# Kernel optimization log

Hardware: AMD Instinct MI355X
Metric: run time of the kernel (lower is better)

## Reference

```python
import jax, jax.numpy as jnp
import numpy as np

B, S, D, H = 2, 2048, 1024, 16
DK = D // H


def setup_inputs() -> dict:
    key = jax.random.key(0)
    ks = jax.random.split(key, 10)
    scale = 1.0 / np.sqrt(D)
    x = jax.random.normal(ks[0], (B, S, D), dtype=jnp.float32)
    # causal mask: 1 = attend, 0 = masked (module's create_causal_mask)
    mask = jnp.tril(jnp.ones((S, S), dtype=jnp.int32))[None, None]
    Wq = jax.random.normal(ks[1], (D, D), jnp.float32) * scale
    bq = jax.random.normal(ks[2], (D,), jnp.float32) * 0.01
    Wk = jax.random.normal(ks[3], (D, D), jnp.float32) * scale
    bk = jax.random.normal(ks[4], (D,), jnp.float32) * 0.01
    Wv = jax.random.normal(ks[5], (D, D), jnp.float32) * scale
    bv = jax.random.normal(ks[6], (D,), jnp.float32) * 0.01
    Wo = jax.random.normal(ks[7], (D, D), jnp.float32) * scale
    bo = jax.random.normal(ks[8], (D,), jnp.float32) * 0.01
    return {"x": x, "mask": mask, "Wq": Wq, "bq": bq, "Wk": Wk, "bk": bk,
            "Wv": Wv, "bv": bv, "Wo": Wo, "bo": bo}


def reference(x, mask, Wq, bq, Wk, bk, Wv, bv, Wo, bo):
    b, s, _ = x.shape
    # projections; [B,S,D] -> [B,H,S,DK]
    def split_heads(t):
        return t.reshape(b, s, H, DK).transpose(0, 2, 1, 3)
    Q = split_heads(x @ Wq + bq)
    K = split_heads(x @ Wk + bk)
    V = split_heads(x @ Wv + bv)
    scores = jnp.einsum('bhqd,bhkd->bhqk', Q, K) / np.sqrt(DK)
    scores = jnp.where(mask == 0, jnp.float32(-1e9), scores)
    attn = jax.nn.softmax(scores, axis=-1)  # dropout p=0 -> identity
    ctx = jnp.einsum('bhqk,bhkd->bhqd', attn, V)
    ctx = ctx.transpose(0, 2, 1, 3).reshape(b, s, D)
    return ctx @ Wo + bo
```

## Files before the change

### kernel.cpp

```cpp
#include <hip/hip_runtime.h>
#include <hip/hip_bf16.h>


typedef _Float16 f16x8 __attribute__((ext_vector_type(8)));
typedef _Float16 f16x4 __attribute__((ext_vector_type(4)));
typedef _Float16 f16x2 __attribute__((ext_vector_type(2)));
typedef float f32x4 __attribute__((ext_vector_type(4)));

#define QSCALE 0.180336880111112f

__device__ __forceinline__ void async_copy16(const _Float16* gsrc,
                                             _Float16* ldst) {
  __builtin_amdgcn_global_load_lds(
      (const __attribute__((address_space(1))) void*)gsrc,
      (__attribute__((address_space(3))) void*)ldst, 16, 0, 0);
}

__global__ __launch_bounds__(256) void prep(
    const float* __restrict__ x, _Float16* __restrict__ xh,
    const float* __restrict__ W0, const float* __restrict__ W1,
    const float* __restrict__ W2, const float* __restrict__ W3,
    _Float16* __restrict__ T0, _Float16* __restrict__ T1,
    _Float16* __restrict__ T2, _Float16* __restrict__ T3) {
  if (blockIdx.x < 4096) {
    int i = (blockIdx.x * 256 + threadIdx.x) * 4;
    float4 v = *(const float4*)(x + i);
    f16x4 o;
    o.x = (_Float16)v.x; o.y = (_Float16)v.y;
    o.z = (_Float16)v.z; o.w = (_Float16)v.w;
    *(f16x4*)(xh + i) = o;
    return;
  }
  const int id = blockIdx.x - 4096;
  const int w = id >> 10, rem = id & 1023;
  const int bx = rem & 31, by = rem >> 5;
  const float* W; _Float16* T;
  switch (w) {
    case 0: W = W0; T = T0; break;
    case 1: W = W1; T = T1; break;
    case 2: W = W2; T = T2; break;
    default: W = W3; T = T3; break;
  }
  __shared__ _Float16 tile[32][33];
  const int tx = threadIdx.x & 31, ty = threadIdx.x >> 5;
  const int n0 = bx * 32, k0 = by * 32;
  for (int i = 0; i < 4; i++) {
    int kk = k0 + ty + i * 8;
    tile[ty + i * 8][tx] = (_Float16)W[(size_t)kk * 1024 + n0 + tx];
  }
  __syncthreads();
  for (int i = 0; i < 4; i++) {
    int nn = n0 + ty + i * 8;
    T[(size_t)nn * 1024 + k0 + tx] = tile[tx][ty + i * 8];
  }
}

__global__ __launch_bounds__(256) void gemm_qkv(
    const _Float16* __restrict__ A, const _Float16* __restrict__ BtAll,
    const float* __restrict__ bq, const float* __restrict__ bk,
    const float* __restrict__ bv, _Float16* __restrict__ Qh,
    _Float16* __restrict__ Kh, _Float16* __restrict__ VT) {
  __shared__ _Float16 As[128 * 32];
  __shared__ _Float16 Bs[128 * 32];
  __shared__ _Float16 tbuf[64 * 136];
  const int tid = threadIdx.x;
  const int wave = tid >> 6, lane = tid & 63;
  const int lr = lane & 15, lq = lane >> 4;
  const int m0 = blockIdx.x * 128, n0 = blockIdx.y * 128;
  const int rw = (wave & 1) * 64, cw = (wave >> 1) * 64;

  const int sel = blockIdx.y >> 3;
  const float* bias = sel == 0 ? bq : (sel == 1 ? bk : bv);
  const int c0 = n0 & 1023;

  f32x4 acc[4][4] = {};
  const int r0 = wave * 32 + (lane >> 2);
  const int woff = (lane & 3) * 8;

  for (int kt = 0; kt < 1024; kt += 32) {
    __syncthreads();
    async_copy16(A + (size_t)(m0 + r0) * 1024 + kt + woff, As + r0 * 32 + woff);
    async_copy16(A + (size_t)(m0 + r0 + 16) * 1024 + kt + woff,
                 As + (r0 + 16) * 32 + woff);
    async_copy16(BtAll + (size_t)(n0 + r0) * 1024 + kt + woff,
                 Bs + r0 * 32 + woff);
    async_copy16(BtAll + (size_t)(n0 + r0 + 16) * 1024 + kt + woff,
                 Bs + (r0 + 16) * 32 + woff);
    __syncthreads();
    f16x8 af[4], bf[4];
    for (int i = 0; i < 4; i++)
      af[i] = *(const f16x8*)(As + (rw + i * 16 + lr) * 32 + lq * 8);
    for (int j = 0; j < 4; j++)
      bf[j] = *(const f16x8*)(Bs + (cw + j * 16 + lr) * 32 + lq * 8);
    for (int i = 0; i < 4; i++)
      for (int j = 0; j < 4; j++)
        acc[i][j] = __builtin_amdgcn_mfma_f32_16x16x32_f16(af[i], bf[j],
                                                           acc[i][j], 0, 0, 0);
  }

  if (sel == 2) {
    const int bb = m0 >> 11, ss0 = m0 & 2047;
    const int cs = tid & 15, dkr = tid >> 4;
    for (int jj = 0; jj < 2; jj++) {
      __syncthreads();
      if ((wave >> 1) == jj) {
        for (int i = 0; i < 4; i++) {
          const int sl = rw + i * 16 + lq * 4;
          for (int j = 0; j < 4; j++) {
            const int dk = j * 16 + lr;
            const float bvl = bias[c0 + jj * 64 + dk];
            f16x4 pv;
            for (int r = 0; r < 4; r++) pv[r] = (_Float16)(acc[i][j][r] + bvl);
            *(f16x4*)(tbuf + dk * 136 + sl) = pv;
          }
        }
      }
      __syncthreads();
      const int hh = (c0 + jj * 64) >> 6;
      _Float16* dst = VT + ((size_t)(bb * 16 + hh) * 64) * 2048 + ss0;
      for (int k = 0; k < 4; k++) {
        const int dk = dkr + k * 16;
        *(uint4*)(dst + (size_t)dk * 2048 + cs * 8) =
            *(const uint4*)(tbuf + dk * 136 + cs * 8);
      }
    }
  } else {
    _Float16* out = sel == 0 ? Qh : Kh;
    const float scl = sel == 0 ? QSCALE : 1.0f;
    for (int i = 0; i < 4; i++) {
      const int row = m0 + rw + i * 16 + lq * 4;
      for (int j = 0; j < 4; j++) {
        const int col = c0 + cw + j * 16 + lr;
        const float bvl = bias[col];
        for (int r = 0; r < 4; r++)
          out[(size_t)(row + r) * 1024 + col] =
              (_Float16)((acc[i][j][r] + bvl) * scl);
      }
    }
  }
}

__global__ __launch_bounds__(256) void gemm_out(
    const _Float16* __restrict__ A, const _Float16* __restrict__ Bt,
    const float* __restrict__ bias, float* __restrict__ out) {
  __shared__ _Float16 As[128 * 32];
  __shared__ _Float16 Bs[64 * 32];
  const int tid = threadIdx.x;
  const int wave = tid >> 6, lane = tid & 63;
  const int lr = lane & 15, lq = lane >> 4;
  const int m0 = blockIdx.x * 128, n0 = blockIdx.y * 64;
  const int rw = (wave & 1) * 64, cw = (wave >> 1) * 32;
  f32x4 acc[4][2] = {};
  const int r0 = wave * 32 + (lane >> 2);
  const int br = tid >> 2;
  const int woff = (lane & 3) * 8;

  for (int kt = 0; kt < 1024; kt += 32) {
    __syncthreads();
    async_copy16(A + (size_t)(m0 + r0) * 1024 + kt + woff, As + r0 * 32 + woff);
    async_copy16(A + (size_t)(m0 + r0 + 16) * 1024 + kt + woff,
                 As + (r0 + 16) * 32 + woff);
    async_copy16(Bt + (size_t)(n0 + br) * 1024 + kt + woff,
                 Bs + br * 32 + woff);
    __syncthreads();
    f16x8 af[4], bf[2];
    for (int i = 0; i < 4; i++)
      af[i] = *(const f16x8*)(As + (rw + i * 16 + lr) * 32 + lq * 8);
    for (int j = 0; j < 2; j++)
      bf[j] = *(const f16x8*)(Bs + (cw + j * 16 + lr) * 32 + lq * 8);
    for (int i = 0; i < 4; i++)
      for (int j = 0; j < 2; j++)
        acc[i][j] = __builtin_amdgcn_mfma_f32_16x16x32_f16(af[i], bf[j],
                                                           acc[i][j], 0, 0, 0);
  }
  for (int i = 0; i < 4; i++) {
    const int row = m0 + rw + i * 16 + lq * 4;
    for (int j = 0; j < 2; j++) {
      const int col = n0 + cw + j * 16 + lr;
      const float bvl = bias[col];
      for (int r = 0; r < 4; r++)
        out[(size_t)(row + r) * 1024 + col] = acc[i][j][r] + bvl;
    }
  }
}

__global__ __launch_bounds__(256) void attn(const _Float16* __restrict__ Q,
                                            const _Float16* __restrict__ K,
                                            const _Float16* __restrict__ VT,
                                            _Float16* __restrict__ ctx) {
  const int qy = blockIdx.y, li = qy & 7;
  int qt;
  switch (qy >> 3) {
    case 0: qt = 31 - li; break;
    case 1: qt = 16 + li; break;
    case 2: qt = 15 - li; break;
    default: qt = li; break;
  }
  const int bh = blockIdx.x;
  const int b = bh >> 4, h = bh & 15;
  const int tid = threadIdx.x, wave = tid >> 6, lane = tid & 63;
  const int lr = lane & 15, lq = lane >> 4;
  const int qmin = qt * 64 + wave * 16;
  const size_t qkbase = ((size_t)b * 2048) * 1024 + h * 64;
  const size_t vtbase = ((size_t)bh) * 64 * 2048;

  __shared__ _Float16 Ks[2][64 * 72];
  __shared__ _Float16 Vs[2][64 * 72];

  const _Float16* qp = Q + qkbase + (size_t)(qmin + lr) * 1024 + lq * 8;
  f16x8 qf0 = *(const f16x8*)qp;
  f16x8 qf1 = *(const f16x8*)(qp + 32);

  f16x4 onesf;
  {
    _Float16 ov = (lr == 0) ? (_Float16)1.0f : (_Float16)0.0f;
    for (int i = 0; i < 4; i++) onesf[i] = ov;
  }

  f32x4 o[4] = {};
  f32x4 ol = {};

  const int sgr = tid >> 2, sgc = (tid & 3) * 8;
  const _Float16* Kg0 = K + qkbase + (size_t)sgr * 1024 + sgc;
  const _Float16* Vg0 = VT + vtbase + (size_t)sgr * 2048 + sgc;
  uint4 ka = *(const uint4*)Kg0, kb = *(const uint4*)(Kg0 + 32);
  uint4 va = *(const uint4*)Vg0, vb = *(const uint4*)(Vg0 + 32);

  for (int t = 0; t <= qt; t++) {
    _Float16* ksb = Ks[t & 1];
    _Float16* vsb = Vs[t & 1];
    *(uint4*)(ksb + sgr * 72 + sgc) = ka;
    *(uint4*)(ksb + sgr * 72 + sgc + 32) = kb;
    *(uint4*)(vsb + sgr * 72 + sgc) = va;
    *(uint4*)(vsb + sgr * 72 + sgc + 32) = vb;
    __syncthreads();
    if (t < qt) {
      const _Float16* kg = Kg0 + (size_t)(t + 1) * 64 * 1024;
      const _Float16* vg = Vg0 + (t + 1) * 64;
      ka = *(const uint4*)kg; kb = *(const uint4*)(kg + 32);
      va = *(const uint4*)vg; vb = *(const uint4*)(vg + 32);
    }

    const int kv0 = t * 64;
    f32x4 s[4];
    for (int ks = 0; ks < 4; ks++) {
      f16x8 k0 = *(const f16x8*)(ksb + (ks * 16 + lr) * 72 + lq * 8);
      f16x8 k1 = *(const f16x8*)(ksb + (ks * 16 + lr) * 72 + 32 + lq * 8);
      f32x4 z = {};
      z = __builtin_amdgcn_mfma_f32_16x16x32_f16(k0, qf0, z, 0, 0, 0);
      z = __builtin_amdgcn_mfma_f32_16x16x32_f16(k1, qf1, z, 0, 0, 0);
      s[ks] = z;
    }
    if (t == qt) {
      const int qcol = qmin + lr;
      for (int ks = 0; ks < 4; ks++)
        for (int r = 0; r < 4; r++)
          if (kv0 + ks * 16 + lq * 4 + r > qcol) s[ks][r] = -1e30f;
    }
    f16x4 pa[4];
    for (int ks = 0; ks < 4; ks++) {
      float p0 = exp2f(s[ks][0]);
      float p1 = exp2f(s[ks][1]);
      float p2 = exp2f(s[ks][2]);
      float p3 = exp2f(s[ks][3]);
      f16x2 q01 = __builtin_bit_cast(f16x2, __builtin_amdgcn_cvt_pkrtz(p0, p1));
      f16x2 q23 = __builtin_bit_cast(f16x2, __builtin_amdgcn_cvt_pkrtz(p2, p3));
      pa[ks] = __builtin_shufflevector(q01, q23, 0, 1, 2, 3);
    }
    for (int ks = 0; ks < 4; ks++) {
      for (int dn = 0; dn < 4; dn++) {
        f16x4 vf =
            *(const f16x4*)(vsb + (dn * 16 + lr) * 72 + ks * 16 + lq * 4);
        o[dn] =
            __builtin_amdgcn_mfma_f32_16x16x16f16(pa[ks], vf, o[dn], 0, 0, 0);
      }
      ol = __builtin_amdgcn_mfma_f32_16x16x16f16(pa[ks], onesf, ol, 0, 0, 0);
    }
  }

  for (int r = 0; r < 4; r++) {
    float lv = __shfl(ol[r], lane & 48);
    float inv = 1.0f / lv;
    const int row = qmin + lq * 4 + r;
    for (int dn = 0; dn < 4; dn++)
      ctx[qkbase + (size_t)row * 1024 + dn * 16 + lr] =
          (_Float16)(o[dn][r] * inv);
  }
}

extern "C" void kernel_launch(void* const* d_in, const int* in_sizes, int n_in,
                              void* d_out, int out_size, void* d_ws,
                              size_t ws_size, hipStream_t stream) {
  const float* x  = (const float*)d_in[0];
  const float* Wq = (const float*)d_in[2];
  const float* bq = (const float*)d_in[3];
  const float* Wk = (const float*)d_in[4];
  const float* bk = (const float*)d_in[5];
  const float* Wv = (const float*)d_in[6];
  const float* bv = (const float*)d_in[7];
  const float* Wo = (const float*)d_in[8];
  const float* bo = (const float*)d_in[9];
  float* out = (float*)d_out;

  char* ws = (char*)d_ws;
  const size_t MB = 1 << 20;
  _Float16* xh  = (_Float16*)(ws);
  _Float16* WTs = (_Float16*)(ws + 8 * MB);
  _Float16* WqT = WTs;
  _Float16* WkT = (_Float16*)(ws + 10 * MB);
  _Float16* WvT = (_Float16*)(ws + 12 * MB);
  _Float16* WoT = (_Float16*)(ws + 14 * MB);
  _Float16* Qh  = (_Float16*)(ws + 16 * MB);
  _Float16* Kh  = (_Float16*)(ws + 24 * MB);
  _Float16* VT  = (_Float16*)(ws + 32 * MB);
  _Float16* ctx = (_Float16*)(ws);

  prep<<<8192, 256, 0, stream>>>(x, xh, Wq, Wk, Wv, Wo, WqT, WkT, WvT, WoT);
  gemm_qkv<<<dim3(32, 24), 256, 0, stream>>>(xh, WTs, bq, bk, bv, Qh, Kh, VT);
  attn<<<dim3(32, 32), 256, 0, stream>>>(Qh, Kh, VT, ctx);
  gemm_out<<<dim3(32, 16), 256, 0, stream>>>(ctx, WoT, bo, out);
}
```

Before: 192.1 us.

## Process 128 query rows per attention block with two 16-row tiles per wave

Each attention workgroup now covers 128 query rows instead of 64, with every wave holding two 16-row Q fragments that share each K/V tile loaded into LDS. This halves the grid and the K/V global-to-LDS traffic per query row. Waves whose rows end before the current KV tile skip its compute, and the PV MFMA section runs under raised wave priority. In exchange, register pressure rises and the causal workload is split more coarsely across fewer blocks, which may reduce occupancy and load balance.

```diff
diff --git a/kernel.cpp b/kernel.cpp
--- a/kernel.cpp
+++ b/kernel.cpp
@@ -188,28 +188,25 @@
                                             const _Float16* __restrict__ K,
                                             const _Float16* __restrict__ VT,
                                             _Float16* __restrict__ ctx) {
-  const int qy = blockIdx.y, li = qy & 7;
-  int qt;
-  switch (qy >> 3) {
-    case 0: qt = 31 - li; break;
-    case 1: qt = 16 + li; break;
-    case 2: qt = 15 - li; break;
-    default: qt = li; break;
-  }
+  const int qy = blockIdx.y;
+  const int j = (qy < 8) ? (15 - qy) : (qy - 8);
   const int bh = blockIdx.x;
   const int b = bh >> 4, h = bh & 15;
   const int tid = threadIdx.x, wave = tid >> 6, lane = tid & 63;
   const int lr = lane & 15, lq = lane >> 4;
-  const int qmin = qt * 64 + wave * 16;
+  const int qmin = j * 128 + wave * 32;
   const size_t qkbase = ((size_t)b * 2048) * 1024 + h * 64;
   const size_t vtbase = ((size_t)bh) * 64 * 2048;
 
   __shared__ _Float16 Ks[2][64 * 72];
   __shared__ _Float16 Vs[2][64 * 72];
 
-  const _Float16* qp = Q + qkbase + (size_t)(qmin + lr) * 1024 + lq * 8;
-  f16x8 qf0 = *(const f16x8*)qp;
-  f16x8 qf1 = *(const f16x8*)(qp + 32);
+  const _Float16* qpA = Q + qkbase + (size_t)(qmin + lr) * 1024 + lq * 8;
+  f16x8 qA0 = *(const f16x8*)qpA;
+  f16x8 qA1 = *(const f16x8*)(qpA + 32);
+  const _Float16* qpB = qpA + (size_t)16 * 1024;
+  f16x8 qB0 = *(const f16x8*)qpB;
+  f16x8 qB1 = *(const f16x8*)(qpB + 32);
 
   f16x4 onesf;
   {
@@ -217,8 +214,8 @@
     for (int i = 0; i < 4; i++) onesf[i] = ov;
   }
 
-  f32x4 o[4] = {};
-  f32x4 ol = {};
+  f32x4 oA[4] = {}, oB[4] = {};
+  f32x4 olA = {}, olB = {};
 
   const int sgr = tid >> 2, sgc = (tid & 3) * 8;
   const _Float16* Kg0 = K + qkbase + (size_t)sgr * 1024 + sgc;
@@ -226,7 +223,10 @@
   uint4 ka = *(const uint4*)Kg0, kb = *(const uint4*)(Kg0 + 32);
   uint4 va = *(const uint4*)Vg0, vb = *(const uint4*)(Vg0 + 32);
 
-  for (int t = 0; t <= qt; t++) {
+  const int tmax = 2 * j + 1;
+  const int myqmax = qmin + 31;
+
+  for (int t = 0; t <= tmax; t++) {
     _Float16* ksb = Ks[t & 1];
     _Float16* vsb = Vs[t & 1];
     *(uint4*)(ksb + sgr * 72 + sgc) = ka;
@@ -234,57 +234,88 @@
     *(uint4*)(vsb + sgr * 72 + sgc) = va;
     *(uint4*)(vsb + sgr * 72 + sgc + 32) = vb;
     __syncthreads();
-    if (t < qt) {
+    if (t < tmax) {
       const _Float16* kg = Kg0 + (size_t)(t + 1) * 64 * 1024;
       const _Float16* vg = Vg0 + (t + 1) * 64;
       ka = *(const uint4*)kg; kb = *(const uint4*)(kg + 32);
       va = *(const uint4*)vg; vb = *(const uint4*)(vg + 32);
     }
-
     const int kv0 = t * 64;
-    f32x4 s[4];
+    if (kv0 > myqmax) continue;
+
+    f32x4 sA[4], sB[4];
     for (int ks = 0; ks < 4; ks++) {
       f16x8 k0 = *(const f16x8*)(ksb + (ks * 16 + lr) * 72 + lq * 8);
       f16x8 k1 = *(const f16x8*)(ksb + (ks * 16 + lr) * 72 + 32 + lq * 8);
-      f32x4 z = {};
-      z = __builtin_amdgcn_mfma_f32_16x16x32_f16(k0, qf0, z, 0, 0, 0);
-      z = __builtin_amdgcn_mfma_f32_16x16x32_f16(k1, qf1, z, 0, 0, 0);
-      s[ks] = z;
-    }
-    if (t == qt) {
+      f32x4 zA = {};
+      zA = __builtin_amdgcn_mfma_f32_16x16x32_f16(k0, qA0, zA, 0, 0, 0);
+      zA = __builtin_amdgcn_mfma_f32_16x16x32_f16(k1, qA1, zA, 0, 0, 0);
+      sA[ks] = zA;
+      f32x4 zB = {};
+      zB = __builtin_amdgcn_mfma_f32_16x16x32_f16(k0, qB0, zB, 0, 0, 0);
+      zB = __builtin_amdgcn_mfma_f32_16x16x32_f16(k1, qB1, zB, 0, 0, 0);
+      sB[ks] = zB;
+    }
+    if (kv0 + 63 > qmin) {
       const int qcol = qmin + lr;
       for (int ks = 0; ks < 4; ks++)
         for (int r = 0; r < 4; r++)
-          if (kv0 + ks * 16 + lq * 4 + r > qcol) s[ks][r] = -1e30f;
-    }
-    f16x4 pa[4];
+          if (kv0 + ks * 16 + lq * 4 + r > qcol) sA[ks][r] = -1e30f;
+    }
+    if (kv0 + 63 > qmin + 16) {
+      const int qcol = qmin + 16 + lr;
+      for (int ks = 0; ks < 4; ks++)
+        for (int r = 0; r < 4; r++)
+          if (kv0 + ks * 16 + lq * 4 + r > qcol) sB[ks][r] = -1e30f;
+    }
+    f16x4 paA[4], paB[4];
     for (int ks = 0; ks < 4; ks++) {
-      float p0 = exp2f(s[ks][0]);
-      float p1 = exp2f(s[ks][1]);
-      float p2 = exp2f(s[ks][2]);
-      float p3 = exp2f(s[ks][3]);
+      float p0 = exp2f(sA[ks][0]);
+      float p1 = exp2f(sA[ks][1]);
+      float p2 = exp2f(sA[ks][2]);
+      float p3 = exp2f(sA[ks][3]);
       f16x2 q01 = __builtin_bit_cast(f16x2, __builtin_amdgcn_cvt_pkrtz(p0, p1));
       f16x2 q23 = __builtin_bit_cast(f16x2, __builtin_amdgcn_cvt_pkrtz(p2, p3));
-      pa[ks] = __builtin_shufflevector(q01, q23, 0, 1, 2, 3);
-    }
+      paA[ks] = __builtin_shufflevector(q01, q23, 0, 1, 2, 3);
+    }
+    for (int ks = 0; ks < 4; ks++) {
+      float p0 = exp2f(sB[ks][0]);
+      float p1 = exp2f(sB[ks][1]);
+      float p2 = exp2f(sB[ks][2]);
+      float p3 = exp2f(sB[ks][3]);
+      f16x2 q01 = __builtin_bit_cast(f16x2, __builtin_amdgcn_cvt_pkrtz(p0, p1));
+      f16x2 q23 = __builtin_bit_cast(f16x2, __builtin_amdgcn_cvt_pkrtz(p2, p3));
+      paB[ks] = __builtin_shufflevector(q01, q23, 0, 1, 2, 3);
+    }
+    __builtin_amdgcn_s_setprio(1);
     for (int ks = 0; ks < 4; ks++) {
       for (int dn = 0; dn < 4; dn++) {
         f16x4 vf =
             *(const f16x4*)(vsb + (dn * 16 + lr) * 72 + ks * 16 + lq * 4);
-        o[dn] =
-            __builtin_amdgcn_mfma_f32_16x16x16f16(pa[ks], vf, o[dn], 0, 0, 0);
+        oA[dn] =
+            __builtin_amdgcn_mfma_f32_16x16x16f16(paA[ks], vf, oA[dn], 0, 0, 0);
+        oB[dn] =
+            __builtin_amdgcn_mfma_f32_16x16x16f16(paB[ks], vf, oB[dn], 0, 0, 0);
       }
-      ol = __builtin_amdgcn_mfma_f32_16x16x16f16(pa[ks], onesf, ol, 0, 0, 0);
-    }
+      olA = __builtin_amdgcn_mfma_f32_16x16x16f16(paA[ks], onesf, olA, 0, 0, 0);
+      olB = __builtin_amdgcn_mfma_f32_16x16x16f16(paB[ks], onesf, olB, 0, 0, 0);
+    }
+    __builtin_amdgcn_s_setprio(0);
   }
 
   for (int r = 0; r < 4; r++) {
-    float lv = __shfl(ol[r], lane & 48);
-    float inv = 1.0f / lv;
-    const int row = qmin + lq * 4 + r;
+    float lvA = __shfl(olA[r], lane & 48);
+    float invA = 1.0f / lvA;
+    const int rowA = qmin + lq * 4 + r;
     for (int dn = 0; dn < 4; dn++)
-      ctx[qkbase + (size_t)row * 1024 + dn * 16 + lr] =
-          (_Float16)(o[dn][r] * inv);
+      ctx[qkbase + (size_t)rowA * 1024 + dn * 16 + lr] =
+          (_Float16)(oA[dn][r] * invA);
+    float lvB = __shfl(olB[r], lane & 48);
+    float invB = 1.0f / lvB;
+    const int rowB = qmin + 16 + lq * 4 + r;
+    for (int dn = 0; dn < 4; dn++)
+      ctx[qkbase + (size_t)rowB * 1024 + dn * 16 + lr] =
+          (_Float16)(oB[dn][r] * invB);
   }
 }
 
@@ -317,6 +348,6 @@
 
   prep<<<8192, 256, 0, stream>>>(x, xh, Wq, Wk, Wv, Wo, WqT, WkT, WvT, WoT);
   gemm_qkv<<<dim3(32, 24), 256, 0, stream>>>(xh, WTs, bq, bk, bv, Qh, Kh, VT);
-  attn<<<dim3(32, 32), 256, 0, stream>>>(Qh, Kh, VT, ctx);
+  attn<<<dim3(32, 16), 256, 0, stream>>>(Qh, Kh, VT, ctx);
   gemm_out<<<dim3(32, 16), 256, 0, stream>>>(ctx, WoT, bo, out);
 }
```

Result: slower. 202.2 us (+5.3%).

## Split KV tile across wave pairs and pair causal q-tiles per block

Applied to the files above, without the earlier changes.

The attention kernel now uses 512-thread blocks where each of four row groups is handled by two waves that split every 64-key tile in half. The two half-results are merged through shared memory before normalisation. Each block processes two query tiles (sp and 31-sp) so causal work is balanced, and MFMA sections get raised wave priority. Wave pairs skip fully masked half-tiles. The cost is an extra shared-memory reduction and more barriers, in exchange for more parallelism per tile and balanced load.

```diff
diff --git a/kernel.cpp b/kernel.cpp
--- a/kernel.cpp
+++ b/kernel.cpp
@@ -184,32 +184,24 @@
   }
 }
 
-__global__ __launch_bounds__(256) void attn(const _Float16* __restrict__ Q,
-                                            const _Float16* __restrict__ K,
-                                            const _Float16* __restrict__ VT,
-                                            _Float16* __restrict__ ctx) {
-  const int qy = blockIdx.y, li = qy & 7;
-  int qt;
-  switch (qy >> 3) {
-    case 0: qt = 31 - li; break;
-    case 1: qt = 16 + li; break;
-    case 2: qt = 15 - li; break;
-    default: qt = li; break;
-  }
+__global__ __launch_bounds__(512, 4) void attn(const _Float16* __restrict__ Q,
+                                               const _Float16* __restrict__ K,
+                                               const _Float16* __restrict__ VT,
+                                               _Float16* __restrict__ ctx) {
+  const int sp = blockIdx.y;
   const int bh = blockIdx.x;
   const int b = bh >> 4, h = bh & 15;
   const int tid = threadIdx.x, wave = tid >> 6, lane = tid & 63;
   const int lr = lane & 15, lq = lane >> 4;
-  const int qmin = qt * 64 + wave * 16;
+  const int rg = wave & 3;
+  const int kvh = wave >> 2;
+  const int kho = kvh * 32;
   const size_t qkbase = ((size_t)b * 2048) * 1024 + h * 64;
   const size_t vtbase = ((size_t)bh) * 64 * 2048;
 
   __shared__ _Float16 Ks[2][64 * 72];
   __shared__ _Float16 Vs[2][64 * 72];
-
-  const _Float16* qp = Q + qkbase + (size_t)(qmin + lr) * 1024 + lq * 8;
-  f16x8 qf0 = *(const f16x8*)qp;
-  f16x8 qf1 = *(const f16x8*)(qp + 32);
+  __shared__ float cb[4 * 64 * 24];
 
   f16x4 onesf;
   {
@@ -217,74 +209,104 @@
     for (int i = 0; i < 4; i++) onesf[i] = ov;
   }
 
-  f32x4 o[4] = {};
-  f32x4 ol = {};
-
-  const int sgr = tid >> 2, sgc = (tid & 3) * 8;
+  const int sgr = tid >> 3, sgc = (tid & 7) * 8;
   const _Float16* Kg0 = K + qkbase + (size_t)sgr * 1024 + sgc;
   const _Float16* Vg0 = VT + vtbase + (size_t)sgr * 2048 + sgc;
-  uint4 ka = *(const uint4*)Kg0, kb = *(const uint4*)(Kg0 + 32);
-  uint4 va = *(const uint4*)Vg0, vb = *(const uint4*)(Vg0 + 32);
-
-  for (int t = 0; t <= qt; t++) {
-    _Float16* ksb = Ks[t & 1];
-    _Float16* vsb = Vs[t & 1];
-    *(uint4*)(ksb + sgr * 72 + sgc) = ka;
-    *(uint4*)(ksb + sgr * 72 + sgc + 32) = kb;
-    *(uint4*)(vsb + sgr * 72 + sgc) = va;
-    *(uint4*)(vsb + sgr * 72 + sgc + 32) = vb;
-    __syncthreads();
-    if (t < qt) {
-      const _Float16* kg = Kg0 + (size_t)(t + 1) * 64 * 1024;
-      const _Float16* vg = Vg0 + (t + 1) * 64;
-      ka = *(const uint4*)kg; kb = *(const uint4*)(kg + 32);
-      va = *(const uint4*)vg; vb = *(const uint4*)(vg + 32);
-    }
-
-    const int kv0 = t * 64;
-    f32x4 s[4];
-    for (int ks = 0; ks < 4; ks++) {
-      f16x8 k0 = *(const f16x8*)(ksb + (ks * 16 + lr) * 72 + lq * 8);
-      f16x8 k1 = *(const f16x8*)(ksb + (ks * 16 + lr) * 72 + 32 + lq * 8);
-      f32x4 z = {};
-      z = __builtin_amdgcn_mfma_f32_16x16x32_f16(k0, qf0, z, 0, 0, 0);
-      z = __builtin_amdgcn_mfma_f32_16x16x32_f16(k1, qf1, z, 0, 0, 0);
-      s[ks] = z;
-    }
-    if (t == qt) {
-      const int qcol = qmin + lr;
-      for (int ks = 0; ks < 4; ks++)
-        for (int r = 0; r < 4; r++)
-          if (kv0 + ks * 16 + lq * 4 + r > qcol) s[ks][r] = -1e30f;
-    }
-    f16x4 pa[4];
-    for (int ks = 0; ks < 4; ks++) {
-      float p0 = exp2f(s[ks][0]);
-      float p1 = exp2f(s[ks][1]);
-      float p2 = exp2f(s[ks][2]);
-      float p3 = exp2f(s[ks][3]);
-      f16x2 q01 = __builtin_bit_cast(f16x2, __builtin_amdgcn_cvt_pkrtz(p0, p1));
-      f16x2 q23 = __builtin_bit_cast(f16x2, __builtin_amdgcn_cvt_pkrtz(p2, p3));
-      pa[ks] = __builtin_shufflevector(q01, q23, 0, 1, 2, 3);
-    }
-    for (int ks = 0; ks < 4; ks++) {
-      for (int dn = 0; dn < 4; dn++) {
-        f16x4 vf =
-            *(const f16x4*)(vsb + (dn * 16 + lr) * 72 + ks * 16 + lq * 4);
-        o[dn] =
-            __builtin_amdgcn_mfma_f32_16x16x16f16(pa[ks], vf, o[dn], 0, 0, 0);
-      }
-      ol = __builtin_amdgcn_mfma_f32_16x16x16f16(pa[ks], onesf, ol, 0, 0, 0);
-    }
-  }
-
-  for (int r = 0; r < 4; r++) {
-    float lv = __shfl(ol[r], lane & 48);
-    float inv = 1.0f / lv;
-    const int row = qmin + lq * 4 + r;
-    for (int dn = 0; dn < 4; dn++)
-      ctx[qkbase + (size_t)row * 1024 + dn * 16 + lr] =
-          (_Float16)(o[dn][r] * inv);
+
+  for (int ph = 0; ph < 2; ph++) {
+    const int st = ph ? 31 - sp : sp;
+    const int qmin = st * 64 + rg * 16;
+    const _Float16* qp = Q + qkbase + (size_t)(qmin + lr) * 1024 + lq * 8;
+    f16x8 qf0 = *(const f16x8*)qp;
+    f16x8 qf1 = *(const f16x8*)(qp + 32);
+    f32x4 o[4] = {};
+    f32x4 ol = {};
+    uint4 ka = *(const uint4*)Kg0;
+    uint4 va = *(const uint4*)Vg0;
+
+    for (int t = 0; t <= st; t++) {
+      _Float16* ksb = Ks[t & 1];
+      _Float16* vsb = Vs[t & 1];
+      *(uint4*)(ksb + sgr * 72 + sgc) = ka;
+      *(uint4*)(vsb + sgr * 72 + sgc) = va;
+      __syncthreads();
+      if (t < st) {
+        const _Float16* kg = Kg0 + (size_t)(t + 1) * 64 * 1024;
+        const _Float16* vg = Vg0 + (t + 1) * 64;
+        ka = *(const uint4*)kg;
+        va = *(const uint4*)vg;
+      }
+      const int kvw = t * 64 + kho;
+      if (kvw > qmin + 15) continue;
+
+      f32x4 s[2];
+      for (int ksl = 0; ksl < 2; ksl++) {
+        const int ksg = kvh * 2 + ksl;
+        f16x8 k0 = *(const f16x8*)(ksb + (ksg * 16 + lr) * 72 + lq * 8);
+        f16x8 k1 = *(const f16x8*)(ksb + (ksg * 16 + lr) * 72 + 32 + lq * 8);
+        f32x4 z = {};
+        z = __builtin_amdgcn_mfma_f32_16x16x32_f16(k0, qf0, z, 0, 0, 0);
+        z = __builtin_amdgcn_mfma_f32_16x16x32_f16(k1, qf1, z, 0, 0, 0);
+        s[ksl] = z;
+      }
+      if (kvw + 31 > qmin) {
+        const int qcol = qmin + lr;
+        for (int ksl = 0; ksl < 2; ksl++)
+          for (int r = 0; r < 4; r++)
+            if (kvw + ksl * 16 + lq * 4 + r > qcol) s[ksl][r] = -1e30f;
+      }
+      f16x4 pa[2];
+      for (int ksl = 0; ksl < 2; ksl++) {
+        float p0 = exp2f(s[ksl][0]);
+        float p1 = exp2f(s[ksl][1]);
+        float p2 = exp2f(s[ksl][2]);
+        float p3 = exp2f(s[ksl][3]);
+        f16x2 q01 =
+            __builtin_bit_cast(f16x2, __builtin_amdgcn_cvt_pkrtz(p0, p1));
+        f16x2 q23 =
+            __builtin_bit_cast(f16x2, __builtin_amdgcn_cvt_pkrtz(p2, p3));
+        pa[ksl] = __builtin_shufflevector(q01, q23, 0, 1, 2, 3);
+      }
+      __builtin_amdgcn_s_setprio(1);
+      for (int ksl = 0; ksl < 2; ksl++) {
+        const int ksg = kvh * 2 + ksl;
+        for (int dn = 0; dn < 4; dn++) {
+          f16x4 vf =
+              *(const f16x4*)(vsb + (dn * 16 + lr) * 72 + ksg * 16 + lq * 4);
+          o[dn] = __builtin_amdgcn_mfma_f32_16x16x16f16(pa[ksl], vf, o[dn], 0,
+                                                        0, 0);
+        }
+        ol = __builtin_amdgcn_mfma_f32_16x16x16f16(pa[ksl], onesf, ol, 0, 0, 0);
+      }
+      __builtin_amdgcn_s_setprio(0);
+    }
+
+    __syncthreads();
+    if (wave >= 4) {
+      float* p = cb + ((wave - 4) * 64 + lane) * 24;
+      *(f32x4*)(p + 0) = o[0];
+      *(f32x4*)(p + 4) = o[1];
+      *(f32x4*)(p + 8) = o[2];
+      *(f32x4*)(p + 12) = o[3];
+      *(f32x4*)(p + 16) = ol;
+    }
+    __syncthreads();
+    if (wave < 4) {
+      const float* p = cb + (wave * 64 + lane) * 24;
+      o[0] += *(const f32x4*)(p + 0);
+      o[1] += *(const f32x4*)(p + 4);
+      o[2] += *(const f32x4*)(p + 8);
+      o[3] += *(const f32x4*)(p + 12);
+      ol += *(const f32x4*)(p + 16);
+      for (int r = 0; r < 4; r++) {
+        float lv = __shfl(ol[r], lane & 48);
+        float inv = 1.0f / lv;
+        const int row = qmin + lq * 4 + r;
+        for (int dn = 0; dn < 4; dn++)
+          ctx[qkbase + (size_t)row * 1024 + dn * 16 + lr] =
+              (_Float16)(o[dn][r] * inv);
+      }
+    }
   }
 }
 
@@ -317,6 +339,6 @@
 
   prep<<<8192, 256, 0, stream>>>(x, xh, Wq, Wk, Wv, Wo, WqT, WkT, WvT, WoT);
   gemm_qkv<<<dim3(32, 24), 256, 0, stream>>>(xh, WTs, bq, bk, bv, Qh, Kh, VT);
-  attn<<<dim3(32, 32), 256, 0, stream>>>(Qh, Kh, VT, ctx);
+  attn<<<dim3(32, 16), 512, 0, stream>>>(Qh, Kh, VT, ctx);
   gemm_out<<<dim3(32, 16), 256, 0, stream>>>(ctx, WoT, bo, out);
 }
```

After: 189.8 us. About the same (-1.2%).
